# Kernel optimization log

Hardware: AMD Instinct MI355X
Metric: run time of the kernel (lower is better)

The kernel has to match this reference:

```python
import jax, jax.numpy as jnp
import numpy as np
import math

N_H = 16

def _rope(x):
    # x: [b, h, n, d_k]; standard RoPE with half-split rotation
    n, d_k = x.shape[2], x.shape[3]
    inv_freq = 1.0 / (10000.0 ** (jnp.arange(0, d_k, 2, dtype=jnp.float32) / d_k))  # [d_k/2]
    freqs = jnp.arange(n, dtype=jnp.float32)[:, None] * inv_freq[None, :]            # [n, d_k/2]
    cos = jnp.concatenate([jnp.cos(freqs), jnp.cos(freqs)], axis=-1)[None, None]     # [1,1,n,d_k]
    sin = jnp.concatenate([jnp.sin(freqs), jnp.sin(freqs)], axis=-1)[None, None]
    x1, x2 = jnp.split(x, 2, axis=-1)
    rot = jnp.concatenate([-x2, x1], axis=-1)
    return x * cos + rot * sin


def setup_inputs() -> dict:
    key = jax.random.key(0)
    k1, k2, k3, k4 = jax.random.split(key, 4)
    b, n, d_m = 2, 1024, 2048
    x = jax.random.normal(k1, (b, n, d_m), dtype=jnp.float32)
    # causal mask (1 = keep, 0 = masked)
    m = jnp.tril(jnp.ones((n, n), dtype=jnp.int32))[None, None]  # [1,1,n,n]
    s = 1.0 / math.sqrt(d_m)
    Wqkv = jax.random.normal(k2, (d_m, 3 * d_m), dtype=jnp.float32) * s
    Wout = jax.random.normal(k3, (d_m, d_m), dtype=jnp.float32) * s
    bout = jax.random.normal(k4, (d_m,), dtype=jnp.float32) * 0.01
    return {"x": x, "m": m, "Wqkv": Wqkv, "Wout": Wout, "bout": bout}


def reference(x, m, Wqkv, Wout, bout):
    b, n, d = x.shape
    d_k = d // N_H
    qkv = (x @ Wqkv).reshape(b, n, 3, N_H, d_k)
    qkv = jnp.transpose(qkv, (2, 0, 3, 1, 4))  # [3, b, h, n, d_k]
    q, k, v = qkv[0], qkv[1], qkv[2]
    q, k = _rope(q), _rope(k)
    s = jnp.einsum('bhqd,bhkd->bhqk', q, k) / math.sqrt(d_k)
    s = jnp.where(m == 0, -jnp.inf, s)
    a = jax.nn.softmax(s, axis=-1)  # dropout is identity in eval / drop=0
    r = jnp.einsum('bhqk,bhkd->bhqd', a, v)
    r = jnp.transpose(r, (0, 2, 1, 3)).reshape(b, n, d)
    return r @ Wout + bout
```

## Files before the change

### kernel.cpp

```cpp
#include <hip/hip_runtime.h>
#include <math.h>

typedef unsigned short u16;
typedef unsigned int u32;
typedef __attribute__((ext_vector_type(8))) short short8;
typedef __attribute__((ext_vector_type(4))) float f32x4;

#define DEVI __device__ __forceinline__

DEVI u16 f2bf(float x) {
    union { float f; u32 u; } un; un.f = x;
    u32 u = un.u;
    return (u16)((u + 0x7fffu + ((u >> 16) & 1u)) >> 16);
}
DEVI u32 cvtpk(float lo, float hi) {
    u32 r;
    asm("v_cvt_pk_bf16_f32 %0, %1, %2" : "=v"(r) : "v"(lo), "v"(hi));
    return r;
}
DEVI float bf2f(u16 v) {
    union { u32 u; float f; } un; un.u = ((u32)v) << 16;
    return un.f;
}
DEVI f32x4 mfma_bf16(short8 a, short8 b, f32x4 c) {
    return __builtin_amdgcn_mfma_f32_16x16x32_bf16(a, b, c, 0, 0, 0);
}
DEVI void gload_lds16(const void* g, void* l) {
    __builtin_amdgcn_global_load_lds((const __attribute__((address_space(1))) u32*)g,
                                     (__attribute__((address_space(3))) u32*)l,
                                     16, 0, 0);
}

__global__ void k_prep(const float* __restrict__ x, const float* __restrict__ Wqkv,
                       const float* __restrict__ Wout, u16* __restrict__ x_bf,
                       u16* __restrict__ WqkvT, u16* __restrict__ WoutT) {
    __shared__ u16 tile[64][68];
    const int bid = blockIdx.x;
    if (bid < 4096) {
        long idx = ((long)bid * 256 + threadIdx.x) * 4;
        float4 v = *(const float4*)(x + idx);
        uint2 o;
        o.x = cvtpk(v.x, v.y);
        o.y = cvtpk(v.z, v.w);
        *(uint2*)(x_bf + idx) = o;
        return;
    }
    const float* in;
    u16* out;
    int R, C, bx, by;
    if (bid < 7168) {
        int lb = bid - 4096;
        in = Wqkv; out = WqkvT; R = 2048; C = 6144;
        bx = lb % 96; by = lb / 96;
    } else {
        int lb = bid - 7168;
        in = Wout; out = WoutT; R = 2048; C = 2048;
        bx = lb & 31; by = lb >> 5;
    }
    const int tx = threadIdx.x & 15, ty = threadIdx.x >> 4;
    const long r0 = (long)by * 64, c0 = (long)bx * 64;
#pragma unroll
    for (int p = 0; p < 4; ++p) {
        int r = ty + p * 16;
        float4 v = *(const float4*)(in + (r0 + r) * C + c0 + tx * 4);
        uint2 o;
        o.x = cvtpk(v.x, v.y);
        o.y = cvtpk(v.z, v.w);
        *(uint2*)&tile[r][tx * 4] = o;
    }
    __syncthreads();
#pragma unroll
    for (int p = 0; p < 4; ++p) {
        int rr = ty + p * 16;
        ushort4 o;
        o.x = tile[tx * 4 + 0][rr];
        o.y = tile[tx * 4 + 1][rr];
        o.z = tile[tx * 4 + 2][rr];
        o.w = tile[tx * 4 + 3][rr];
        *(ushort4*)(out + (c0 + rr) * R + r0 + tx * 4) = o;
    }
}

template <int EPI, int TM>
__global__ __launch_bounds__(256, 3) void k_gemm(const u16* __restrict__ A,
                                                 const u16* __restrict__ BT, int K,
                                                 u16* __restrict__ qb, u16* __restrict__ kb,
                                                 u16* __restrict__ vtb, float* __restrict__ out,
                                                 const float* __restrict__ bias) {
    constexpr int MI = TM / 32;
    constexpr int CA = TM / 32;
    __shared__ __align__(16) union SM {
        struct { u16 As[TM * 64]; u16 Bs[128 * 64]; } s;
        u16 T[EPI == 0 ? 128 * 132 : 8];
    } sm;
    const int tid = threadIdx.x;
    const int lane = tid & 63, wave = tid >> 6;
    const int lm = lane & 15, quad = lane >> 4;
    const int wm = wave >> 1, wn = wave & 1;
    const int nwg = gridDim.x * gridDim.y;
    const int lin = blockIdx.y * gridDim.x + blockIdx.x;
    const int work = (lin & 7) * (nwg >> 3) + (lin >> 3);
    const int bm = work % gridDim.x, bn = work / gridDim.x;

    f32x4 acc[MI][4] = {};

    const int srow = lane >> 3;
    const int scb = (lane & 7) ^ srow;
    const long arow0 = (long)bm * TM;
    const long brow0 = (long)bn * 128;

    for (int k0 = 0; k0 < K; k0 += 64) {
        __syncthreads();
#pragma unroll
        for (int it = 0; it < CA; ++it) {
            int ch = wave * CA + it;
            long r = ch * 8 + srow;
            gload_lds16(A + (arow0 + r) * K + k0 + scb * 8, (char*)sm.s.As + ch * 1024);
        }
#pragma unroll
        for (int it = 0; it < 4; ++it) {
            int ch = wave * 4 + it;
            long r = ch * 8 + srow;
            gload_lds16(BT + (brow0 + r) * K + k0 + scb * 8, (char*)sm.s.Bs + ch * 1024);
        }
        __syncthreads();
#pragma unroll
        for (int ko = 0; ko < 2; ++ko) {
            short8 af[MI], bf[4];
#pragma unroll
            for (int i = 0; i < MI; ++i) {
                int row = wm * (TM / 2) + i * 16 + lm;
                int pc = (ko * 4 + quad) ^ (lm & 7);
                af[i] = *(const short8*)&sm.s.As[row * 64 + pc * 8];
            }
#pragma unroll
            for (int j = 0; j < 4; ++j) {
                int row = wn * 64 + j * 16 + lm;
                int pc = (ko * 4 + quad) ^ (lm & 7);
                bf[j] = *(const short8*)&sm.s.Bs[row * 64 + pc * 8];
            }
#pragma unroll
            for (int i = 0; i < MI; ++i)
#pragma unroll
                for (int j = 0; j < 4; ++j)
                    acc[i][j] = mfma_bf16(af[i], bf[j], acc[i][j]);
        }
    }

    if constexpr (EPI == 0) {
        __syncthreads();
#pragma unroll
        for (int i = 0; i < MI; ++i)
#pragma unroll
            for (int j = 0; j < 4; ++j) {
                const int col = wn * 64 + j * 16 + lm;
                const int row0 = wm * 64 + i * 16 + quad * 4;
                const u32 p01 = cvtpk(acc[i][j][0], acc[i][j][1]);
                const u32 p23 = cvtpk(acc[i][j][2], acc[i][j][3]);
                sm.T[(row0 + 0) * 132 + col] = (u16)p01;
                sm.T[(row0 + 1) * 132 + col] = (u16)(p01 >> 16);
                sm.T[(row0 + 2) * 132 + col] = (u16)p23;
                sm.T[(row0 + 3) * 132 + col] = (u16)(p23 >> 16);
            }
        __syncthreads();
        const int which = bn >> 4, h = bn & 15, b = bm >> 3;
        const int p0 = (bm & 7) * 128;
        if (which < 2) {
            u16* dst = which ? kb : qb;
            const long hb = ((long)(b * 16 + h)) * 1024;
            const int i0 = (tid * 4) & 63;
            const int pb = tid >> 4;
            float inv[4];
#pragma unroll
            for (int e = 0; e < 4; ++e)
                inv[e] = exp2f(-(float)(i0 + e) * 0.20762050593045952f);
#pragma unroll
            for (int c = 0; c < 8; ++c) {
                const int pos_l = c * 16 + pb;
                ushort4 cur = *(const ushort4*)&sm.T[pos_l * 132 + i0];
                ushort4 par = *(const ushort4*)&sm.T[pos_l * 132 + i0 + 64];
                const float pg = (float)(p0 + pos_l);
                const u16* cp = (const u16*)&cur;
                const u16* pp = (const u16*)&par;
                float f1[4], f2[4];
#pragma unroll
                for (int e = 0; e < 4; ++e) {
                    float th = pg * inv[e];
                    float sv = __sinf(th), cv = __cosf(th);
                    float x1 = bf2f(cp[e]), x2 = bf2f(pp[e]);
                    f1[e] = x1 * cv - x2 * sv;
                    f2[e] = x2 * cv + x1 * sv;
                }
                uint2 o1, o2;
                o1.x = cvtpk(f1[0], f1[1]); o1.y = cvtpk(f1[2], f1[3]);
                o2.x = cvtpk(f2[0], f2[1]); o2.y = cvtpk(f2[2], f2[3]);
                const long rowb = (hb + p0 + pos_l) * 128;
                *(uint2*)(dst + rowb + i0) = o1;
                *(uint2*)(dst + rowb + i0 + 64) = o2;
            }
        } else {
            const long vrow = ((long)(b * 16 + h)) * 128;
#pragma unroll
            for (int c = 0; c < 8; ++c) {
                const int lin2 = c * 2048 + tid * 8;
                const int dk = lin2 >> 7;
                const int ps = lin2 & 127;
                ushort4 o1, o2;
                u16* o1p = (u16*)&o1;
                u16* o2p = (u16*)&o2;
#pragma unroll
                for (int e = 0; e < 4; ++e) {
                    o1p[e] = sm.T[(ps + e) * 132 + dk];
                    o2p[e] = sm.T[(ps + 4 + e) * 132 + dk];
                }
                u16* dst = vtb + (vrow + dk) * 1024 + p0 + ps;
                *(ushort4*)dst = o1;
                *(ushort4*)(dst + 4) = o2;
            }
        }
    } else {
        float bv[4];
#pragma unroll
        for (int j = 0; j < 4; ++j) bv[j] = bias[bn * 128 + wn * 64 + j * 16 + lm];
#pragma unroll
        for (int i = 0; i < MI; ++i) {
#pragma unroll
            for (int r = 0; r < 4; ++r) {
                const int row = bm * TM + wm * (TM / 2) + i * 16 + quad * 4 + r;
#pragma unroll
                for (int j = 0; j < 4; ++j) {
                    const int col = bn * 128 + wn * 64 + j * 16 + lm;
                    out[(long)row * 2048 + col] = acc[i][j][r] + bv[j];
                }
            }
        }
    }
}

__global__ __launch_bounds__(256, 3) void k_out(const u16* __restrict__ A,
                                                const u16* __restrict__ BT,
                                                float* __restrict__ out,
                                                const float* __restrict__ bias) {
    __shared__ __align__(16) struct { u16 As[128 * 64]; u16 Bs[128 * 64]; } sm;
    const int tid = threadIdx.x;
    const int lane = tid & 63, wave = tid >> 6;
    const int lm = lane & 15, quad = lane >> 4;
    const int wm = wave >> 1, wn = wave & 1;
    const int b = blockIdx.x;
    const int z = (b >> 3) & 1;
    const int p = (b >> 4) * 8 + (b & 7);
    const int bm = p & 15, bn = p >> 4;

    f32x4 acc[4][4] = {};
    const int srow = lane >> 3;
    const int scb = (lane & 7) ^ srow;
    const long arow0 = (long)bm * 128;
    const long brow0 = (long)bn * 128;
    const int koff = z * 1024;

    for (int k0 = 0; k0 < 1024; k0 += 64) {
        __syncthreads();
#pragma unroll
        for (int it = 0; it < 4; ++it) {
            int ch = wave * 4 + it;
            long r = ch * 8 + srow;
            gload_lds16(A + (arow0 + r) * 2048 + koff + k0 + scb * 8,
                        (char*)sm.As + ch * 1024);
            gload_lds16(BT + (brow0 + r) * 2048 + koff + k0 + scb * 8,
                        (char*)sm.Bs + ch * 1024);
        }
        __syncthreads();
#pragma unroll
        for (int ko = 0; ko < 2; ++ko) {
            short8 af[4], bf[4];
#pragma unroll
            for (int i = 0; i < 4; ++i) {
                int row = wm * 64 + i * 16 + lm;
                int pc = (ko * 4 + quad) ^ (lm & 7);
                af[i] = *(const short8*)&sm.As[row * 64 + pc * 8];
            }
#pragma unroll
            for (int j = 0; j < 4; ++j) {
                int row = wn * 64 + j * 16 + lm;
                int pc = (ko * 4 + quad) ^ (lm & 7);
                bf[j] = *(const short8*)&sm.Bs[row * 64 + pc * 8];
            }
#pragma unroll
            for (int i = 0; i < 4; ++i)
#pragma unroll
                for (int j = 0; j < 4; ++j)
                    acc[i][j] = mfma_bf16(af[i], bf[j], acc[i][j]);
        }
    }

    float bv[4];
#pragma unroll
    for (int j = 0; j < 4; ++j)
        bv[j] = z ? 0.f : bias[bn * 128 + wn * 64 + j * 16 + lm];
#pragma unroll
    for (int i = 0; i < 4; ++i) {
#pragma unroll
        for (int r = 0; r < 4; ++r) {
            const long row = bm * 128 + wm * 64 + i * 16 + quad * 4 + r;
#pragma unroll
            for (int j = 0; j < 4; ++j) {
                const int col = bn * 128 + wn * 64 + j * 16 + lm;
                atomicAdd(&out[row * 2048 + col], acc[i][j][r] + bv[j]);
            }
        }
    }
}

__global__ __launch_bounds__(256, 2) void k_flash(const u16* __restrict__ Q,
                                                  const u16* __restrict__ Kb,
                                                  const u16* __restrict__ VT,
                                                  u16* __restrict__ R) {
    __shared__ u16 Ks[2][64 * 128];
    __shared__ u16 Vs[2][128 * 64];
    __shared__ u16 Ps[64 * 72];
    const int tid = threadIdx.x;
    const int lane = tid & 63, wave = tid >> 6;
    const int lm = lane & 15, quad = lane >> 4;
    const int p = blockIdx.x;
    const int half = p >> 8, q8 = p & 255;
    const int xcd = q8 & 7, j8 = q8 >> 3;
    const int bh = xcd * 4 + (j8 >> 3);
    const int s = j8 & 7;
    const int qt = half ? (15 - s) : s;
    const long qkbase = (long)bh * 1024 * 128;
    const long vtbase = (long)bh * 128 * 1024;
    const int q0 = qt * 64;

    short8 qf[4];
    {
        const u16* qrow = Q + qkbase + (long)(q0 + wave * 16 + lm) * 128 + quad * 8;
#pragma unroll
        for (int kc = 0; kc < 4; ++kc) qf[kc] = *(const short8*)(qrow + kc * 32);
    }

    f32x4 o_acc[8] = {};
    float m_i = -INFINITY, l_i = 0.f;
    const float cl2e = 0.08838834764831845f * 1.4426950408889634f;

    const int kr = lane >> 4;
    const int vr = lane >> 3;
    const int vcb = (lane & 7) ^ vr;

    auto stage = [&](int buf, int kt) {
#pragma unroll
        for (int it = 0; it < 4; ++it) {
            int ch = wave * 4 + it;
            int krow = ch * 4 + kr;
            int kchunk = (lane & 15) ^ (krow & 15);
            gload_lds16(Kb + qkbase + (long)(kt * 64 + krow) * 128 + kchunk * 8,
                        (char*)Ks[buf] + ch * 1024);
            int vrow = ch * 8 + vr;
            gload_lds16(VT + vtbase + (long)vrow * 1024 + kt * 64 + vcb * 8,
                        (char*)Vs[buf] + ch * 1024);
        }
    };

    stage(0, 0);
    __syncthreads();
    int cur = 0;

    for (int kt = 0; kt <= qt; ++kt) {
        if (kt < qt) stage(cur ^ 1, kt + 1);
        asm volatile("" ::: "memory");

        f32x4 s_acc[4] = {};
        __builtin_amdgcn_s_setprio(1);
#pragma unroll
        for (int kc = 0; kc < 4; ++kc) {
#pragma unroll
            for (int mi = 0; mi < 4; ++mi) {
                int row = mi * 16 + lm;
                int pc = (kc * 4 + quad) ^ lm;
                short8 ak = *(const short8*)&Ks[cur][row * 128 + pc * 8];
                s_acc[mi] = mfma_bf16(ak, qf[kc], s_acc[mi]);
            }
        }
        __builtin_amdgcn_s_setprio(0);
        float t[4][4];
        float cmax = -INFINITY;
        if (kt < qt) {
#pragma unroll
            for (int mi = 0; mi < 4; ++mi)
#pragma unroll
                for (int r = 0; r < 4; ++r) {
                    float val = s_acc[mi][r] * cl2e;
                    t[mi][r] = val;
                    cmax = fmaxf(cmax, val);
                }
        } else {
            const int qg = q0 + wave * 16 + lm;
#pragma unroll
            for (int mi = 0; mi < 4; ++mi)
#pragma unroll
                for (int r = 0; r < 4; ++r) {
                    int kg = kt * 64 + mi * 16 + quad * 4 + r;
                    float val = (kg <= qg) ? s_acc[mi][r] * cl2e : -INFINITY;
                    t[mi][r] = val;
                    cmax = fmaxf(cmax, val);
                }
        }
        cmax = fmaxf(cmax, __shfl_xor(cmax, 16));
        cmax = fmaxf(cmax, __shfl_xor(cmax, 32));
        float m_new = fmaxf(m_i, cmax);
        const bool defer = __all(cmax - m_i <= 8.f);
        if (defer) m_new = m_i;
        float csum = 0.f;
#pragma unroll
        for (int mi = 0; mi < 4; ++mi)
#pragma unroll
            for (int r = 0; r < 4; ++r) {
                float p2 = exp2f(t[mi][r] - m_new);
                t[mi][r] = p2;
                csum += p2;
            }
        csum += __shfl_xor(csum, 16);
        csum += __shfl_xor(csum, 32);
        if (!defer) {
            float alpha = exp2f(m_i - m_new);
            float aq[4];
#pragma unroll
            for (int r = 0; r < 4; ++r) aq[r] = __shfl(alpha, quad * 4 + r, 64);
#pragma unroll
            for (int nt = 0; nt < 8; ++nt)
#pragma unroll
                for (int r = 0; r < 4; ++r) o_acc[nt][r] *= aq[r];
            l_i = l_i * alpha + csum;
        } else {
            l_i += csum;
        }
        m_i = m_new;
#pragma unroll
        for (int mi = 0; mi < 4; ++mi) {
            uint2 pk2;
            pk2.x = cvtpk(t[mi][0], t[mi][1]);
            pk2.y = cvtpk(t[mi][2], t[mi][3]);
            *(uint2*)&Ps[(wave * 16 + lm) * 72 + mi * 16 + quad * 4] = pk2;
        }
        __builtin_amdgcn_s_setprio(1);
#pragma unroll
        for (int kc = 0; kc < 2; ++kc) {
            short8 ap = *(const short8*)&Ps[(wave * 16 + lm) * 72 + kc * 32 + quad * 8];
#pragma unroll
            for (int nt = 0; nt < 8; ++nt) {
                int row = nt * 16 + lm;
                int pc = (kc * 4 + quad) ^ (lm & 7);
                short8 bv = *(const short8*)&Vs[cur][row * 64 + pc * 8];
                o_acc[nt] = mfma_bf16(ap, bv, o_acc[nt]);
            }
        }
        __builtin_amdgcn_s_setprio(0);
        __syncthreads();
        cur ^= 1;
    }
    float lq[4], il[4];
#pragma unroll
    for (int r = 0; r < 4; ++r) lq[r] = __shfl(l_i, quad * 4 + r, 64);
#pragma unroll
    for (int r = 0; r < 4; ++r) il[r] = 1.0f / lq[r];
    u16* Os = (u16*)Ks;
    const int row0 = wave * 16 + quad * 4;
#pragma unroll
    for (int nt = 0; nt < 8; ++nt) {
        const u32 p01 = cvtpk(o_acc[nt][0] * il[0], o_acc[nt][1] * il[1]);
        const u32 p23 = cvtpk(o_acc[nt][2] * il[2], o_acc[nt][3] * il[3]);
        const int col = nt * 16 + lm;
        Os[(row0 + 0) * 136 + col] = (u16)p01;
        Os[(row0 + 1) * 136 + col] = (u16)(p01 >> 16);
        Os[(row0 + 2) * 136 + col] = (u16)p23;
        Os[(row0 + 3) * 136 + col] = (u16)(p23 >> 16);
    }
    __syncthreads();
    const int b = bh >> 4, h = bh & 15;
    const long rbase = ((long)b * 1024 + q0) * 2048 + h * 128;
    const int rr = tid >> 4, c0 = (tid & 15) * 8;
#pragma unroll
    for (int pass = 0; pass < 4; ++pass) {
        const int row = pass * 16 + rr;
        *(uint4*)(R + rbase + (long)row * 2048 + c0) = *(const uint4*)&Os[row * 136 + c0];
    }
}

extern "C" void kernel_launch(void* const* d_in, const int* in_sizes, int n_in,
                              void* d_out, int out_size, void* d_ws, size_t ws_size,
                              hipStream_t stream) {
    const float* x    = (const float*)d_in[0];
    const float* Wqkv = (const float*)d_in[2];
    const float* Wout = (const float*)d_in[3];
    const float* bout = (const float*)d_in[4];
    float* out = (float*)d_out;

    char* ws = (char*)d_ws;
    u16* x_bf  = (u16*)(ws);
    u16* rbuf  = x_bf;
    u16* WqkvT = (u16*)(ws + (8L << 20));
    u16* WoutT = (u16*)(ws + (32L << 20));
    u16* qbuf  = (u16*)(ws + (40L << 20));
    u16* kbuf  = (u16*)(ws + (48L << 20));
    u16* vtbuf = (u16*)(ws + (56L << 20));

    hipMemsetAsync(out, 0, (size_t)2048 * 2048 * sizeof(float), stream);
    k_prep<<<8192, 256, 0, stream>>>(x, Wqkv, Wout, x_bf, WqkvT, WoutT);
    k_gemm<0, 128><<<dim3(16, 48), 256, 0, stream>>>(x_bf, WqkvT, 2048, qbuf, kbuf, vtbuf,
                                                     nullptr, nullptr);
    k_flash<<<512, 256, 0, stream>>>(qbuf, kbuf, vtbuf, rbuf);
    k_out<<<512, 256, 0, stream>>>(rbuf, WoutT, out, bout);
}
```

Before: 257.2 us.

## Replace split-K atomic accumulation with partial buffers and a combine kernel

The output projection's two K-halves now store plain float partial results into two workspace buffers, instead of atomically adding into a zeroed output. A new elementwise kernel sums the two partials and adds the bias, which also removes the up-front memset of the output. The block-to-work mapping is changed so each group of eight consecutive launch indices spreads its work across XCDs in contiguous chunks. The trade is float atomics plus a memset against extra global traffic and one more kernel launch. The partial buffers reuse workspace regions whose earlier contents are already consumed.

```diff
diff --git a/kernel.cpp b/kernel.cpp
--- a/kernel.cpp
+++ b/kernel.cpp
@@ -239,16 +239,17 @@
 
 __global__ __launch_bounds__(256, 3) void k_out(const u16* __restrict__ A,
                                                 const u16* __restrict__ BT,
-                                                float* __restrict__ out,
-                                                const float* __restrict__ bias) {
+                                                float* __restrict__ p0f,
+                                                float* __restrict__ p1f) {
     __shared__ __align__(16) struct { u16 As[128 * 64]; u16 Bs[128 * 64]; } sm;
     const int tid = threadIdx.x;
     const int lane = tid & 63, wave = tid >> 6;
     const int lm = lane & 15, quad = lane >> 4;
     const int wm = wave >> 1, wn = wave & 1;
-    const int b = blockIdx.x;
-    const int z = (b >> 3) & 1;
-    const int p = (b >> 4) * 8 + (b & 7);
+    const int lin = blockIdx.x;
+    const int work = (lin & 7) * 64 + (lin >> 3);
+    const int z = work >> 8;
+    const int p = work & 255;
     const int bm = p & 15, bn = p >> 4;
 
     f32x4 acc[4][4] = {};
@@ -293,10 +294,7 @@
         }
     }
 
-    float bv[4];
-#pragma unroll
-    for (int j = 0; j < 4; ++j)
-        bv[j] = z ? 0.f : bias[bn * 128 + wn * 64 + j * 16 + lm];
+    float* dst = z ? p1f : p0f;
 #pragma unroll
     for (int i = 0; i < 4; ++i) {
 #pragma unroll
@@ -305,10 +303,24 @@
 #pragma unroll
             for (int j = 0; j < 4; ++j) {
                 const int col = bn * 128 + wn * 64 + j * 16 + lm;
-                atomicAdd(&out[row * 2048 + col], acc[i][j][r] + bv[j]);
-            }
-        }
-    }
+                dst[row * 2048 + col] = acc[i][j][r];
+            }
+        }
+    }
+}
+
+__global__ void k_comb(const float* __restrict__ p0f, const float* __restrict__ p1f,
+                       const float* __restrict__ bias, float* __restrict__ out) {
+    const long i = ((long)blockIdx.x * 256 + threadIdx.x) * 4;
+    float4 a = *(const float4*)(p0f + i);
+    float4 b = *(const float4*)(p1f + i);
+    float4 bv = *(const float4*)(bias + (i & 2047));
+    float4 o;
+    o.x = a.x + b.x + bv.x;
+    o.y = a.y + b.y + bv.y;
+    o.z = a.z + b.z + bv.z;
+    o.w = a.w + b.w + bv.w;
+    *(float4*)(out + i) = o;
 }
 
 __global__ __launch_bounds__(256, 2) void k_flash(const u16* __restrict__ Q,
@@ -502,11 +514,13 @@
     u16* qbuf  = (u16*)(ws + (40L << 20));
     u16* kbuf  = (u16*)(ws + (48L << 20));
     u16* vtbuf = (u16*)(ws + (56L << 20));
-
-    hipMemsetAsync(out, 0, (size_t)2048 * 2048 * sizeof(float), stream);
+    float* p0f = (float*)(ws + (8L << 20));
+    float* p1f = (float*)(ws + (40L << 20));
+
     k_prep<<<8192, 256, 0, stream>>>(x, Wqkv, Wout, x_bf, WqkvT, WoutT);
     k_gemm<0, 128><<<dim3(16, 48), 256, 0, stream>>>(x_bf, WqkvT, 2048, qbuf, kbuf, vtbuf,
                                                      nullptr, nullptr);
     k_flash<<<512, 256, 0, stream>>>(qbuf, kbuf, vtbuf, rbuf);
-    k_out<<<512, 256, 0, stream>>>(rbuf, WoutT, out, bout);
-}
+    k_out<<<512, 256, 0, stream>>>(rbuf, WoutT, p0f, p1f);
+    k_comb<<<4096, 256, 0, stream>>>(p0f, p1f, bout, out);
+}
```

Result: faster. 241.0 us (-6.3%).
